# Optimization experiments

Measured on AMD Instinct MI355X. Metric: run time of the kernel, lower is better.

The kernel has to match this reference:

```python
import jax, jax.numpy as jnp
import numpy as np


def setup_inputs() -> dict:
    key = jax.random.key(0)
    k0, k1, k2, k3 = jax.random.split(key, 4)
    B, H, W, C = 2, 128, 128, 512
    N_SPIX = 256  # (H/8)*(W/8) superpixels on an 8-px grid
    x = jax.random.normal(k0, (B, H, W, C), jnp.float32)
    sims = jax.random.uniform(k1, (B, H, W, 9), jnp.float32)
    sinds = jax.random.randint(k2, (B, H, W, 9), 0, N_SPIX, jnp.int32)
    W_qk = jax.random.normal(k3, (C, 2 * C), jnp.float32) * 0.02
    b_qk = jnp.zeros((2 * C,), jnp.float32)
    return {"x": x, "sims": sims, "sinds": sinds, "W_qk": W_qk, "b_qk": b_qk,
            "kernel_size": 7, "num_heads": 4}


def reference(x, sims, sinds, W_qk, b_qk, kernel_size, num_heads):
    """Soft-neighborhood superpixel attention scores.

    attn[b,g,si,h,w,ki] = <q[b,g,h,w], k[b,g,hj,wj]> + log p_j(s)
    where (hj,wj) is the ki-th pixel of the clamped (NATTEN-style) KxK window
    around (h,w), s = sinds[b,h,w,si] is the si-th neighboring-superpixel id
    of pixel (h,w), and p_j(s) = sum_m sims[b,hj,wj,m] * [sinds[b,hj,wj,m]==s]
    (the soft probability that key pixel j belongs to superpixel s; entries
    where s is not among j's 9 neighbor superpixels stay at -inf, matching
    the -inf-initialized attn buffer of the CUDA kernel).
    """
    B, H, W, C = x.shape
    K = kernel_size
    hd = C // num_heads
    r = K // 2

    # qk projection -> (B, heads, H, W, hd) for q and k (permute(3,0,4,1,2,5))
    qk = (x @ W_qk + b_qk).reshape(B, H, W, 2, num_heads, hd)
    q = jnp.moveaxis(qk[:, :, :, 0], 3, 1)  # (B,HD,H,W,hd)
    k = jnp.moveaxis(qk[:, :, :, 1], 3, 1)

    # NATTEN clamped window starts
    hs = jnp.clip(jnp.arange(H) - r, 0, H - K)  # (H,)
    ws = jnp.clip(jnp.arange(W) - r, 0, W - K)  # (W,)
    s_i = sinds  # (B,H,W,9): superpixel ids of pixel i's 9 neighbors

    dots, logps = [], []
    for dh in range(K):
        hj = hs + dh  # (H,)
        for dw in range(K):
            wj = ws + dw  # (W,)
            # gather key/sims/sinds at window offset (dh,dw)
            k_off = k[:, :, hj[:, None], wj[None, :], :]        # (B,HD,H,W,hd)
            dots.append(jnp.einsum('bghwf,bghwf->bghw', q, k_off))
            sind_j = sinds[:, hj[:, None], wj[None, :], :]      # (B,H,W,9)
            sim_j = sims[:, hj[:, None], wj[None, :], :]        # (B,H,W,9)
            # p_j(s_i): match i's si-th superpixel against j's 9 ids
            match = sind_j[:, :, :, None, :] == s_i[:, :, :, :, None]  # (B,H,W,9si,9m)
            pj = jnp.sum(jnp.where(match, sim_j[:, :, :, None, :], 0.0), axis=-1)  # (B,H,W,9)
            logps.append(jnp.where(pj > 0, jnp.log(jnp.maximum(pj, 1e-30)), -jnp.inf))

    dots = jnp.stack(dots, axis=-1)            # (B,HD,H,W,K*K)
    logp = jnp.stack(logps, axis=-1)           # (B,H,W,9,K*K)
    logp = jnp.moveaxis(logp, 3, 1)            # (B,9,H,W,K*K)
    attn = dots[:, :, None] + logp[:, None]    # (B,HD,9,H,W,K*K)
    return attn
```

## Files before the change

### kernel.cpp

```cpp
#include <hip/hip_runtime.h>
#include <hip/hip_bf16.h>
#include <math.h>

#define BATCH 2
#define HH 128
#define WW 128
#define CC 512
#define NH 4
#define HD 128
#define KS 7
#define RR 3
#define KK2 49
#define NSI 9

#define GM (BATCH*HH*WW)
#define GK CC
#define GN (2*CC)

#define NEG_HUGE (-1.0e30f)

typedef __attribute__((ext_vector_type(8))) short bf16x8;
typedef __attribute__((ext_vector_type(4))) float f32x4;

__device__ __forceinline__ float sout(float v) {
    return fminf(fmaxf(v, -3.0e38f), 3.0e38f);
}
__device__ __forceinline__ float bflo(unsigned int u) {
    return __builtin_bit_cast(float, u << 16);
}
__device__ __forceinline__ float bfhi(unsigned int u) {
    return __builtin_bit_cast(float, u & 0xffff0000u);
}
__device__ __forceinline__ unsigned short f2bf(float f) {
    unsigned int u = __builtin_bit_cast(unsigned int, f);
    u += 0x7fffu + ((u >> 16) & 1u);
    return (unsigned short)(u >> 16);
}

__device__ __forceinline__ void gl_lds16(const unsigned short* g, unsigned short* l) {
    __builtin_amdgcn_global_load_lds(
        (const __attribute__((address_space(1))) unsigned int*)g,
        (__attribute__((address_space(3))) unsigned int*)l, 16, 0, 0);
}

__global__ __launch_bounds__(256) void xcast(const float* __restrict__ x,
                                             unsigned short* __restrict__ xb) {
    int t = blockIdx.x * 256 + threadIdx.x;
    const float4* s = (const float4*)(x + (size_t)t * 8);
    float4 v0 = s[0], v1 = s[1];
    bf16x8 pk;
    pk[0] = (short)f2bf(v0.x); pk[1] = (short)f2bf(v0.y);
    pk[2] = (short)f2bf(v0.z); pk[3] = (short)f2bf(v0.w);
    pk[4] = (short)f2bf(v1.x); pk[5] = (short)f2bf(v1.y);
    pk[6] = (short)f2bf(v1.z); pk[7] = (short)f2bf(v1.w);
    *(bf16x8*)(xb + (size_t)t * 8) = pk;
}

__global__ __launch_bounds__(256) void wtrans(const float* __restrict__ W,
                                              unsigned short* __restrict__ Wt) {
    int t = blockIdx.x * 256 + threadIdx.x;
    int n = t >> 9, k = t & 511;
    Wt[(size_t)n * GK + k] = f2bf(W[(size_t)k * GN + n]);
}

#define TBM 128
#define TBN 128
#define TBK 64

__global__ __launch_bounds__(256, 2) void qk_gemm_async(
        const unsigned short* __restrict__ xb,
        const unsigned short* __restrict__ Wt,
        const float* __restrict__ bias,
        unsigned short* __restrict__ Cout)
{
    __shared__ unsigned short As[TBM * TBK];
    __shared__ unsigned short Bs[TBN * TBK];

    const int m0 = blockIdx.x * TBM;
    const int n0 = blockIdx.y * TBN;
    const int tid = threadIdx.x;
    const int lane = tid & 63;
    const int wid = tid >> 6;
    const int wr = wid >> 1, wc = wid & 1;

    f32x4 acc[4][4];
#pragma unroll
    for (int i = 0; i < 4; ++i)
#pragma unroll
        for (int j = 0; j < 4; ++j) acc[i][j] = (f32x4){0.f, 0.f, 0.f, 0.f};

    const int srow = lane >> 3;
    const int scol = (lane & 7) * 8;

    for (int k0 = 0; k0 < GK; k0 += TBK) {
#pragma unroll
        for (int i = 0; i < 4; ++i) {
            int chunk = wid * 4 + i;
            int row = chunk * 8 + srow;
            gl_lds16(xb + (size_t)(m0 + row) * GK + k0 + scol, &As[chunk * 512]);
            gl_lds16(Wt + (size_t)(n0 + row) * GK + k0 + scol, &Bs[chunk * 512]);
        }
        __syncthreads();

#pragma unroll
        for (int ks = 0; ks < 2; ++ks) {
            const int koff = ks * 32 + (lane >> 4) * 8;
            bf16x8 af[4], bfr[4];
#pragma unroll
            for (int i = 0; i < 4; ++i)
                af[i] = *(const bf16x8*)&As[(wr * 64 + i * 16 + (lane & 15)) * TBK + koff];
#pragma unroll
            for (int j = 0; j < 4; ++j)
                bfr[j] = *(const bf16x8*)&Bs[(wc * 64 + j * 16 + (lane & 15)) * TBK + koff];
#pragma unroll
            for (int i = 0; i < 4; ++i)
#pragma unroll
                for (int j = 0; j < 4; ++j)
                    acc[i][j] = __builtin_amdgcn_mfma_f32_16x16x32_bf16(
                        af[i], bfr[j], acc[i][j], 0, 0, 0);
        }
        __syncthreads();
    }

    const int colbase = n0 + wc * 64;
    float bias4[4];
#pragma unroll
    for (int j = 0; j < 4; ++j) bias4[j] = bias[colbase + j * 16 + (lane & 15)];
#pragma unroll
    for (int i = 0; i < 4; ++i) {
#pragma unroll
        for (int j = 0; j < 4; ++j) {
#pragma unroll
            for (int r = 0; r < 4; ++r) {
                int row = m0 + wr * 64 + i * 16 + (lane >> 4) * 4 + r;
                int col = colbase + j * 16 + (lane & 15);
                Cout[(size_t)row * GN + col] = f2bf(acc[i][j][r] + bias4[j]);
            }
        }
    }
}

#define LDAB 72

__global__ __launch_bounds__(256) void qk_gemm_conv(
        const float* __restrict__ X,
        const unsigned short* __restrict__ Wt,
        const float* __restrict__ bias,
        unsigned short* __restrict__ Cout)
{
    __shared__ unsigned short As[TBM][LDAB];
    __shared__ unsigned short Bs[TBN][LDAB];

    const int m0 = blockIdx.x * TBM;
    const int n0 = blockIdx.y * TBN;
    const int tid = threadIdx.x;
    const int lane = tid & 63;
    const int wid = tid >> 6;
    const int wr = wid >> 1, wc = wid & 1;

    f32x4 acc[4][4];
#pragma unroll
    for (int i = 0; i < 4; ++i)
#pragma unroll
        for (int j = 0; j < 4; ++j) acc[i][j] = (f32x4){0.f, 0.f, 0.f, 0.f};

    const int srow = tid >> 1;
    const int shalf = (tid & 1) * 32;

    for (int k0 = 0; k0 < GK; k0 += TBK) {
        {
            const float* srcA = X + (size_t)(m0 + srow) * GK + k0 + shalf;
#pragma unroll
            for (int i = 0; i < 4; ++i) {
                float4 v0 = ((const float4*)srcA)[i * 2];
                float4 v1 = ((const float4*)srcA)[i * 2 + 1];
                bf16x8 pk;
                pk[0] = (short)f2bf(v0.x); pk[1] = (short)f2bf(v0.y);
                pk[2] = (short)f2bf(v0.z); pk[3] = (short)f2bf(v0.w);
                pk[4] = (short)f2bf(v1.x); pk[5] = (short)f2bf(v1.y);
                pk[6] = (short)f2bf(v1.z); pk[7] = (short)f2bf(v1.w);
                *(bf16x8*)&As[srow][shalf + i * 8] = pk;
            }
        }
        {
            const unsigned short* srcB = Wt + (size_t)(n0 + srow) * GK + k0 + shalf;
#pragma unroll
            for (int i = 0; i < 4; ++i)
                *(uint4*)&Bs[srow][shalf + i * 8] = ((const uint4*)srcB)[i];
        }
        __syncthreads();

#pragma unroll
        for (int ks = 0; ks < 2; ++ks) {
            const int koff = ks * 32 + (lane >> 4) * 8;
            bf16x8 af[4], bfr[4];
#pragma unroll
            for (int i = 0; i < 4; ++i)
                af[i] = *(const bf16x8*)&As[wr * 64 + i * 16 + (lane & 15)][koff];
#pragma unroll
            for (int j = 0; j < 4; ++j)
                bfr[j] = *(const bf16x8*)&Bs[wc * 64 + j * 16 + (lane & 15)][koff];
#pragma unroll
            for (int i = 0; i < 4; ++i)
#pragma unroll
                for (int j = 0; j < 4; ++j)
                    acc[i][j] = __builtin_amdgcn_mfma_f32_16x16x32_bf16(
                        af[i], bfr[j], acc[i][j], 0, 0, 0);
        }
        __syncthreads();
    }

    const int colbase = n0 + wc * 64;
    float bias4[4];
#pragma unroll
    for (int j = 0; j < 4; ++j) bias4[j] = bias[colbase + j * 16 + (lane & 15)];
#pragma unroll
    for (int i = 0; i < 4; ++i)
#pragma unroll
        for (int j = 0; j < 4; ++j)
#pragma unroll
            for (int r = 0; r < 4; ++r) {
                int row = m0 + wr * 64 + i * 16 + (lane >> 4) * 4 + r;
                int col = colbase + j * 16 + (lane & 15);
                Cout[(size_t)row * GN + col] = f2bf(acc[i][j][r] + bias4[j]);
            }
}

#define HALO 14
#define LQK 136
#define LSS 212
#define NIT 13
#define NITEMS (64*KK2)

__global__ __launch_bounds__(256) void attn_mfma(
        const unsigned short* __restrict__ qk,
        const float* __restrict__ sims,
        const int*   __restrict__ sinds,
        float* __restrict__ out)
{
    __shared__ __align__(16) unsigned char smem[73984];
    unsigned short* Qs = (unsigned short*)smem;
    unsigned short* Ks = (unsigned short*)(smem + 17408);
    float* Ss = (float*)smem;

    const int tw = blockIdx.x, th = blockIdx.y, b = blockIdx.z;
    const int tid = threadIdx.x;
    const int lane = tid & 63;
    const int wm = tid >> 6;

    const int h0 = th * 8, w0 = tw * 8;
    const int hb = min(max(h0 - RR, 0), HH - KS);
    const int wb = min(max(w0 - RR, 0), WW - KS);

    float dacc[NIT][NH];

#pragma unroll
    for (int g = 0; g < NH; ++g) {
#pragma unroll
        for (int p = 0; p < 4; ++p) {
            int o = tid + p * 256;
            int pl = o >> 4, c = o & 15;
            int h = h0 + (pl >> 3), w = w0 + (pl & 7);
            size_t base = ((size_t)((b * HH + h) * WW + w)) * GN + g * HD + c * 8;
            *(uint4*)&Qs[pl * LQK + c * 8] = *(const uint4*)(qk + base);
        }
#pragma unroll
        for (int p = 0; p < 13; ++p) {
            int o = tid + p * 256;
            int jj = o >> 4, c = o & 15;
            int jr = min(jj, HALO * HALO - 1);
            int hj = min(hb + jr / HALO, HH - 1);
            int wj = min(wb + jr % HALO, WW - 1);
            size_t base = ((size_t)((b * HH + hj) * WW + wj)) * GN + CC + g * HD + c * 8;
            *(uint4*)&Ks[jj * LQK + c * 8] = *(const uint4*)(qk + base);
        }
        __syncthreads();

        const int koff = (lane >> 4) * 8;
        bf16x8 aq[4];
#pragma unroll
        for (int ks = 0; ks < 4; ++ks)
            aq[ks] = *(const bf16x8*)&Qs[(wm * 16 + (lane & 15)) * LQK + ks * 32 + koff];

        f32x4 svals[13];
#pragma unroll
        for (int nt = 0; nt < 13; ++nt) {
            f32x4 sacc = (f32x4){0.f, 0.f, 0.f, 0.f};
#pragma unroll
            for (int ks = 0; ks < 4; ++ks) {
                bf16x8 bk = *(const bf16x8*)&Ks[(nt * 16 + (lane & 15)) * LQK + ks * 32 + koff];
                sacc = __builtin_amdgcn_mfma_f32_16x16x32_bf16(aq[ks], bk, sacc, 0, 0, 0);
            }
            svals[nt] = sacc;
        }
        __syncthreads();

#pragma unroll
        for (int nt = 0; nt < 13; ++nt)
#pragma unroll
            for (int r = 0; r < 4; ++r) {
                int qrow = wm * 16 + (lane >> 4) * 4 + r;
                Ss[qrow * LSS + nt * 16 + (lane & 15)] = svals[nt][r];
            }
        __syncthreads();

#pragma unroll
        for (int r = 0; r < NIT; ++r) {
            int it = tid + r * 256;
            if (it < NITEMS) {
                int pl = it / KK2, ki = it % KK2;
                int h = h0 + (pl >> 3), w = w0 + (pl & 7);
                int dh = ki / KS, dw = ki % KS;
                int hj = min(max(h - RR, 0), HH - KS) + dh;
                int wj = min(max(w - RR, 0), WW - KS) + dw;
                int j = (hj - hb) * HALO + (wj - wb);
                dacc[r][g] = Ss[pl * LSS + j];
            }
        }
        __syncthreads();
    }

    const size_t plane = (size_t)HH * WW * KK2;
#pragma unroll
    for (int r = 0; r < NIT; ++r) {
        int it = tid + r * 256;
        if (it < NITEMS) {
            int pl = it / KK2, ki = it % KK2;
            int h = h0 + (pl >> 3), w = w0 + (pl & 7);
            int dh = ki / KS, dw = ki % KS;
            int hj = min(max(h - RR, 0), HH - KS) + dh;
            int wj = min(max(w - RR, 0), WW - KS) + dw;
            int pix = (b * HH + h) * WW + w;
            int pj  = (b * HH + hj) * WW + wj;

            int sid[NSI], sjd[NSI]; float sjm[NSI];
            const int*   sip = sinds + (size_t)pix * NSI;
            const int*   sjp = sinds + (size_t)pj * NSI;
            const float* smp = sims + (size_t)pj * NSI;
#pragma unroll
            for (int m = 0; m < NSI; ++m) { sid[m] = sip[m]; sjd[m] = sjp[m]; sjm[m] = smp[m]; }

            float lp[NSI];
#pragma unroll
            for (int si = 0; si < NSI; ++si) {
                float p = 0.f;
#pragma unroll
                for (int m = 0; m < NSI; ++m) p += (sjd[m] == sid[si]) ? sjm[m] : 0.f;
                lp[si] = (p > 0.f) ? __logf(fmaxf(p, 1e-30f)) : NEG_HUGE;
            }

            size_t inner = (size_t)(h * WW + w) * KK2 + ki;
#pragma unroll
            for (int g = 0; g < NH; ++g)
#pragma unroll
                for (int si = 0; si < NSI; ++si)
                    out[((size_t)((b * NH + g) * NSI + si)) * plane + inner] =
                        sout(dacc[r][g] + lp[si]);
        }
    }
}

#define FT 8
#define FH 14
#define FNP (FT*FT)
#define FNJ (FH*FH)
#define FDH 64
#define KPAD 68
#define FNITEM (FNP*KK2)
#define FNR 13

__global__ __launch_bounds__(256) void fused_attn(
        const float* __restrict__ x, const float* __restrict__ sims,
        const int* __restrict__ sinds, const float* __restrict__ Wm,
        const float* __restrict__ bias, float* __restrict__ out)
{
    __shared__ unsigned short kt[FNJ][KPAD];
    __shared__ unsigned short qt[FNP][KPAD];

    const int tw = blockIdx.x, th = blockIdx.y;
    const int b = blockIdx.z >> 2, g = blockIdx.z & 3;
    const int tid = threadIdx.x;
    const int hb = min(max(th * FT - RR, 0), HH - KS);
    const int wb = min(max(tw * FT - RR, 0), WW - KS);

    float dacc[FNR];
#pragma unroll
    for (int r = 0; r < FNR; ++r) dacc[r] = 0.f;

    for (int ph = 0; ph < 2; ++ph) {
        const int kcol0 = CC + g * HD + ph * FDH;
        const int qcol0 = g * HD + ph * FDH;

        for (int o = tid; o < FNJ * FDH; o += 256) {
            int j = o >> 6, dd = o & 63;
            int hj = min(hb + j / FH, HH - 1), wj = min(wb + j % FH, WW - 1);
            const float* xr = x + ((size_t)(b * HH + hj) * WW + wj) * CC;
            int col = kcol0 + dd;
            float acc = bias[col];
            for (int c = 0; c < CC; c += 4) {
                float4 xv = *(const float4*)(xr + c);
                acc += xv.x * Wm[(size_t)c * GN + col]
                     + xv.y * Wm[(size_t)(c + 1) * GN + col]
                     + xv.z * Wm[(size_t)(c + 2) * GN + col]
                     + xv.w * Wm[(size_t)(c + 3) * GN + col];
            }
            kt[j][dd] = f2bf(acc);
        }
        for (int o = tid; o < FNP * FDH; o += 256) {
            int i = o >> 6, dd = o & 63;
            int h = th * FT + (i >> 3), w = tw * FT + (i & 7);
            const float* xr = x + ((size_t)(b * HH + h) * WW + w) * CC;
            int col = qcol0 + dd;
            float acc = bias[col];
            for (int c = 0; c < CC; c += 4) {
                float4 xv = *(const float4*)(xr + c);
                acc += xv.x * Wm[(size_t)c * GN + col]
                     + xv.y * Wm[(size_t)(c + 1) * GN + col]
                     + xv.z * Wm[(size_t)(c + 2) * GN + col]
                     + xv.w * Wm[(size_t)(c + 3) * GN + col];
            }
            qt[i][dd] = f2bf(acc);
        }
        __syncthreads();

#pragma unroll
        for (int r = 0; r < FNR; ++r) {
            int it = tid + r * 256;
            if (it < FNITEM) {
                int pl = it / KK2, ki = it % KK2;
                int h = th * FT + (pl >> 3), w = tw * FT + (pl & 7);
                int dh = ki / KS, dw = ki % KS;
                int hj = min(max(h - RR, 0), HH - KS) + dh;
                int wj = min(max(w - RR, 0), WW - KS) + dw;
                int j = (hj - hb) * FH + (wj - wb);
                const unsigned int* qr = (const unsigned int*)&qt[pl][0];
                const unsigned int* kr = (const unsigned int*)&kt[j][0];
                float a = 0.f;
#pragma unroll 8
                for (int d = 0; d < FDH / 2; ++d) {
                    unsigned int qv = qr[d], kv = kr[d];
                    a += bflo(qv) * bflo(kv) + bfhi(qv) * bfhi(kv);
                }
                dacc[r] += a;
            }
        }
        __syncthreads();
    }

    const size_t plane = (size_t)HH * WW * KK2;
#pragma unroll
    for (int r = 0; r < FNR; ++r) {
        int it = tid + r * 256;
        if (it < FNITEM) {
            int pl = it / KK2, ki = it % KK2;
            int h = th * FT + (pl >> 3), w = tw * FT + (pl & 7);
            int dh = ki / KS, dw = ki % KS;
            int hj = min(max(h - RR, 0), HH - KS) + dh;
            int wj = min(max(w - RR, 0), WW - KS) + dw;
            int pix = (b * HH + h) * WW + w;
            int pj  = (b * HH + hj) * WW + wj;

            int sid[NSI], sjd[NSI]; float sjm[NSI];
            const int*   sip = sinds + (size_t)pix * NSI;
            const int*   sjp = sinds + (size_t)pj * NSI;
            const float* smp = sims + (size_t)pj * NSI;
#pragma unroll
            for (int m = 0; m < NSI; ++m) { sid[m] = sip[m]; sjd[m] = sjp[m]; sjm[m] = smp[m]; }

            const size_t inner = (size_t)(h * WW + w) * KK2 + ki;
#pragma unroll
            for (int si = 0; si < NSI; ++si) {
                float p = 0.f;
#pragma unroll
                for (int m = 0; m < NSI; ++m) p += (sjd[m] == sid[si]) ? sjm[m] : 0.f;
                float lp = (p > 0.f) ? __logf(fmaxf(p, 1e-30f)) : NEG_HUGE;
                out[((size_t)((b * NH + g) * NSI + si)) * plane + inner] =
                    sout(dacc[r] + lp);
            }
        }
    }
}

extern "C" void kernel_launch(void* const* d_in, const int* in_sizes, int n_in,
                              void* d_out, int out_size, void* d_ws, size_t ws_size,
                              hipStream_t stream) {
    const float* x     = (const float*)d_in[0];
    const float* sims  = (const float*)d_in[1];
    const int*   sinds = (const int*)d_in[2];
    const float* W_qk  = (const float*)d_in[3];
    const float* b_qk  = (const float*)d_in[4];
    float* out = (float*)d_out;

    const size_t qk_bytes = (size_t)GM * GN * sizeof(unsigned short);
    const size_t wt_bytes = (size_t)GN * GK * sizeof(unsigned short);
    const size_t xb_bytes = (size_t)GM * GK * sizeof(unsigned short);

    dim3 ggrid(GM / TBM, GN / TBN);
    dim3 agrid(WW / 8, HH / 8, BATCH);

    if (ws_size >= qk_bytes + wt_bytes + xb_bytes) {
        unsigned short* qk = (unsigned short*)d_ws;
        unsigned short* Wt = (unsigned short*)((char*)d_ws + qk_bytes);
        unsigned short* xb = (unsigned short*)((char*)d_ws + qk_bytes + wt_bytes);

        wtrans<<<(GK * GN) / 256, 256, 0, stream>>>(W_qk, Wt);
        xcast<<<(GM * GK) / (256 * 8), 256, 0, stream>>>(x, xb);
        qk_gemm_async<<<ggrid, 256, 0, stream>>>(xb, Wt, b_qk, qk);
        attn_mfma<<<agrid, 256, 0, stream>>>(qk, sims, sinds, out);
    } else if (ws_size >= qk_bytes + wt_bytes) {
        unsigned short* qk = (unsigned short*)d_ws;
        unsigned short* Wt = (unsigned short*)((char*)d_ws + qk_bytes);

        wtrans<<<(GK * GN) / 256, 256, 0, stream>>>(W_qk, Wt);
        qk_gemm_conv<<<ggrid, 256, 0, stream>>>(x, Wt, b_qk, qk);
        attn_mfma<<<agrid, 256, 0, stream>>>(qk, sims, sinds, out);
    } else {
        dim3 fgrid(WW / FT, HH / FT, BATCH * NH);
        fused_attn<<<fgrid, 256, 0, stream>>>(x, sims, sinds, W_qk, b_qk, out);
    }
}
```

Baseline: 194.3 us.

## Prefetch K tiles into registers across heads, load Q directly, retune occupancy

The attention kernel now loads Q fragments straight from global memory instead of staging them in shared memory. It also prefetches the next head's K halo tile into registers while the current head's MFMA scores are computed, which shrinks the shared-memory footprint and targets two blocks per CU. Separately, the GEMM grid is swapped so blocks sharing an M tile run adjacently, and its occupancy hint is raised to 3. The register prefetch adds register pressure, which could cause spills under the tighter launch bounds.

```diff
diff --git a/kernel.cpp b/kernel.cpp
--- a/kernel.cpp
+++ b/kernel.cpp
@@ -67,7 +67,7 @@
 #define TBN 128
 #define TBK 64
 
-__global__ __launch_bounds__(256, 2) void qk_gemm_async(
+__global__ __launch_bounds__(256, 3) void qk_gemm_async(
         const unsigned short* __restrict__ xb,
         const unsigned short* __restrict__ Wt,
         const float* __restrict__ bias,
@@ -76,8 +76,8 @@
     __shared__ unsigned short As[TBM * TBK];
     __shared__ unsigned short Bs[TBN * TBK];
 
-    const int m0 = blockIdx.x * TBM;
-    const int n0 = blockIdx.y * TBN;
+    const int n0 = blockIdx.x * TBN;
+    const int m0 = blockIdx.y * TBM;
     const int tid = threadIdx.x;
     const int lane = tid & 63;
     const int wid = tid >> 6;
@@ -127,17 +127,15 @@
 #pragma unroll
     for (int j = 0; j < 4; ++j) bias4[j] = bias[colbase + j * 16 + (lane & 15)];
 #pragma unroll
-    for (int i = 0; i < 4; ++i) {
-#pragma unroll
-        for (int j = 0; j < 4; ++j) {
+    for (int i = 0; i < 4; ++i)
+#pragma unroll
+        for (int j = 0; j < 4; ++j)
 #pragma unroll
             for (int r = 0; r < 4; ++r) {
                 int row = m0 + wr * 64 + i * 16 + (lane >> 4) * 4 + r;
                 int col = colbase + j * 16 + (lane & 15);
                 Cout[(size_t)row * GN + col] = f2bf(acc[i][j][r] + bias4[j]);
             }
-        }
-    }
 }
 
 #define LDAB 72
@@ -232,15 +230,14 @@
 #define NIT 13
 #define NITEMS (64*KK2)
 
-__global__ __launch_bounds__(256) void attn_mfma(
+__global__ __launch_bounds__(256, 2) void attn_mfma(
         const unsigned short* __restrict__ qk,
         const float* __restrict__ sims,
         const int*   __restrict__ sinds,
         float* __restrict__ out)
 {
-    __shared__ __align__(16) unsigned char smem[73984];
-    unsigned short* Qs = (unsigned short*)smem;
-    unsigned short* Ks = (unsigned short*)(smem + 17408);
+    __shared__ __align__(16) unsigned char smem[208 * LQK * 2];
+    unsigned short* Ks = (unsigned short*)smem;
     float* Ss = (float*)smem;
 
     const int tw = blockIdx.x, th = blockIdx.y, b = blockIdx.z;
@@ -252,55 +249,69 @@
     const int hb = min(max(h0 - RR, 0), HH - KS);
     const int wb = min(max(w0 - RR, 0), WW - KS);
 
+    unsigned int koff32[NIT];
+    int jjv[NIT], ccv[NIT];
+#pragma unroll
+    for (int p = 0; p < NIT; ++p) {
+        int o = tid + p * 256;
+        int jj = o >> 4, c = o & 15;
+        int jr = min(jj, HALO * HALO - 1);
+        int hj = min(hb + jr / HALO, HH - 1);
+        int wj = min(wb + jr % HALO, WW - 1);
+        koff32[p] = (unsigned int)((((b * HH + hj) * WW + wj) * GN + CC + c * 8) * 2);
+        jjv[p] = jj; ccv[p] = c;
+    }
+
+    const int pl_q = wm * 16 + (lane & 15);
+    const size_t qrow = ((size_t)(b * HH + h0 + (pl_q >> 3)) * WW + w0 + (pl_q & 7)) * GN;
+    const int kof8 = (lane >> 4) * 8;
+
+    uint4 kbuf[NIT];
+#pragma unroll
+    for (int p = 0; p < NIT; ++p)
+        kbuf[p] = *(const uint4*)((const char*)qk + koff32[p]);
+
     float dacc[NIT][NH];
 
 #pragma unroll
     for (int g = 0; g < NH; ++g) {
-#pragma unroll
-        for (int p = 0; p < 4; ++p) {
-            int o = tid + p * 256;
-            int pl = o >> 4, c = o & 15;
-            int h = h0 + (pl >> 3), w = w0 + (pl & 7);
-            size_t base = ((size_t)((b * HH + h) * WW + w)) * GN + g * HD + c * 8;
-            *(uint4*)&Qs[pl * LQK + c * 8] = *(const uint4*)(qk + base);
-        }
-#pragma unroll
-        for (int p = 0; p < 13; ++p) {
-            int o = tid + p * 256;
-            int jj = o >> 4, c = o & 15;
-            int jr = min(jj, HALO * HALO - 1);
-            int hj = min(hb + jr / HALO, HH - 1);
-            int wj = min(wb + jr % HALO, WW - 1);
-            size_t base = ((size_t)((b * HH + hj) * WW + wj)) * GN + CC + g * HD + c * 8;
-            *(uint4*)&Ks[jj * LQK + c * 8] = *(const uint4*)(qk + base);
-        }
-        __syncthreads();
-
-        const int koff = (lane >> 4) * 8;
         bf16x8 aq[4];
 #pragma unroll
         for (int ks = 0; ks < 4; ++ks)
-            aq[ks] = *(const bf16x8*)&Qs[(wm * 16 + (lane & 15)) * LQK + ks * 32 + koff];
-
-        f32x4 svals[13];
-#pragma unroll
-        for (int nt = 0; nt < 13; ++nt) {
+            aq[ks] = *(const bf16x8*)(qk + qrow + g * HD + ks * 32 + kof8);
+
+#pragma unroll
+        for (int p = 0; p < NIT; ++p)
+            *(uint4*)&Ks[jjv[p] * LQK + ccv[p] * 8] = kbuf[p];
+        __syncthreads();
+
+        if (g < NH - 1) {
+#pragma unroll
+            for (int p = 0; p < NIT; ++p)
+                kbuf[p] = *(const uint4*)((const char*)qk + koff32[p] + (g + 1) * 256);
+        }
+
+        __builtin_amdgcn_s_setprio(1);
+        f32x4 svals[NIT];
+#pragma unroll
+        for (int nt = 0; nt < NIT; ++nt) {
             f32x4 sacc = (f32x4){0.f, 0.f, 0.f, 0.f};
 #pragma unroll
             for (int ks = 0; ks < 4; ++ks) {
-                bf16x8 bk = *(const bf16x8*)&Ks[(nt * 16 + (lane & 15)) * LQK + ks * 32 + koff];
+                bf16x8 bk = *(const bf16x8*)&Ks[(nt * 16 + (lane & 15)) * LQK + ks * 32 + kof8];
                 sacc = __builtin_amdgcn_mfma_f32_16x16x32_bf16(aq[ks], bk, sacc, 0, 0, 0);
             }
             svals[nt] = sacc;
         }
-        __syncthreads();
-
-#pragma unroll
-        for (int nt = 0; nt < 13; ++nt)
+        __builtin_amdgcn_s_setprio(0);
+        __syncthreads();
+
+#pragma unroll
+        for (int nt = 0; nt < NIT; ++nt)
 #pragma unroll
             for (int r = 0; r < 4; ++r) {
-                int qrow = wm * 16 + (lane >> 4) * 4 + r;
-                Ss[qrow * LSS + nt * 16 + (lane & 15)] = svals[nt][r];
+                int qr = wm * 16 + (lane >> 4) * 4 + r;
+                Ss[qr * LSS + nt * 16 + (lane & 15)] = svals[nt][r];
             }
         __syncthreads();
 
@@ -495,7 +506,6 @@
     const size_t wt_bytes = (size_t)GN * GK * sizeof(unsigned short);
     const size_t xb_bytes = (size_t)GM * GK * sizeof(unsigned short);
 
-    dim3 ggrid(GM / TBM, GN / TBN);
     dim3 agrid(WW / 8, HH / 8, BATCH);
 
     if (ws_size >= qk_bytes + wt_bytes + xb_bytes) {
@@ -505,6 +515,7 @@
 
         wtrans<<<(GK * GN) / 256, 256, 0, stream>>>(W_qk, Wt);
         xcast<<<(GM * GK) / (256 * 8), 256, 0, stream>>>(x, xb);
+        dim3 ggrid(GN / TBN, GM / TBM);
         qk_gemm_async<<<ggrid, 256, 0, stream>>>(xb, Wt, b_qk, qk);
         attn_mfma<<<agrid, 256, 0, stream>>>(qk, sims, sinds, out);
     } else if (ws_size >= qk_bytes + wt_bytes) {
@@ -512,6 +523,7 @@
         unsigned short* Wt = (unsigned short*)((char*)d_ws + qk_bytes);
 
         wtrans<<<(GK * GN) / 256, 256, 0, stream>>>(W_qk, Wt);
+        dim3 ggrid(GM / TBM, GN / TBN);
         qk_gemm_conv<<<ggrid, 256, 0, stream>>>(x, Wt, b_qk, qk);
         attn_mfma<<<agrid, 256, 0, stream>>>(qk, sims, sinds, out);
     } else {
```

Measured after the change: 195.0 us. No clear change (+0.3%).
